# Performance work log

Measured on AMD Instinct MI355X. Metric: run time of the kernel, lower is better.

The kernel has to match this reference:

```python
import jax, jax.numpy as jnp
import numpy as np

N, E, R, D = 50000, 100000, 64, 50


def setup_inputs() -> dict:
    key = jax.random.key(0)
    k0, k1, k2, k3, k4 = jax.random.split(key, 5)
    h = jax.random.normal(k0, (N, D), dtype=jnp.float32)
    # xavier_uniform with gain=sqrt(2) (relu): bound = gain*sqrt(6/(fan_in+fan_out))
    bound = np.sqrt(2.0) * np.sqrt(6.0 / (D + D))
    weight = jax.random.uniform(k1, (R, D, D), dtype=jnp.float32, minval=-bound, maxval=bound)
    bias = jnp.ones((D,), dtype=jnp.float32)
    src_idx = jax.random.randint(k2, (E,), 0, N)
    dst_idx = jax.random.randint(k3, (E,), 0, N)
    rel_type = jax.random.randint(k4, (E,), 0, R)
    return {"h": h, "weight": weight, "bias": bias,
            "src_idx": src_idx, "dst_idx": dst_idx, "rel_type": rel_type}


def reference(h, weight, bias, src_idx, dst_idx, rel_type):
    # message_func: per-edge relation weight gather + bmm with source features
    # h[src_idx]: [E, D], weight[rel_type]: [E, D, D] -> msg: [E, D]
    msg = jnp.einsum('ed,edk->ek', h[src_idx], weight[rel_type])
    # sum-reduce messages onto destination nodes (DGL fn.sum semantics)
    agg = jax.ops.segment_sum(msg, dst_idx, num_segments=N)
    # apply_func: bias add + ReLU on node features
    return jax.nn.relu(agg + bias)
```

## Files before the change

kernel.cpp:

```cpp
#include <hip/hip_runtime.h>

#define NN 50000
#define DD 50
#define RR 64
#define BINS 2048
#define CAP 128
#define CAPN 24

#define BINCUR_OFF 0
#define DCUR_OFF   2048
#define PERM_OFF   52048
#define SD_OFF     1252048
#define META_INTS  1776336
#define WB_BYTE    ((size_t)META_INTS * 4)
#define HB_BYTE    ((WB_BYTE + (size_t)RR * 64 * 64 * 2 + 127) & ~(size_t)127)
#define MSG_BYTE   (HB_BYTE + (size_t)NN * 64 * 2)
#define WS_NEED    (MSG_BYTE + (size_t)BINS * CAP * 64 * 2)

typedef __attribute__((ext_vector_type(8))) short bf16x8;
typedef __attribute__((ext_vector_type(4))) float f32x4;

__device__ __forceinline__ unsigned short f2b(float f) {
    unsigned u = __float_as_uint(f);
    u = (u + 0x7fffu + ((u >> 16) & 1u)) >> 16;
    return (unsigned short)u;
}

__global__ __launch_bounds__(256) void k_init(int* __restrict__ meta,
        unsigned short* __restrict__ wb, unsigned short* __restrict__ hb,
        const float* __restrict__ w, const float* __restrict__ h) {
    int tid = blockIdx.x * 256 + threadIdx.x;
    int nth = gridDim.x * 256;
    for (int j = tid; j < BINS + NN; j += nth) meta[j] = 0;
    for (int j = tid; j < RR * 64 * 64; j += nth) {
        int r = j >> 12, n = (j >> 6) & 63, d = j & 63;
        float v = (n < DD && d < DD) ? w[r * (DD * DD) + d * DD + n] : 0.f;
        wb[j] = f2b(v);
    }
    for (int j = tid; j < NN * 32; j += nth) {
        int n = j >> 5, cp = j & 31;
        unsigned pack = 0;
        if (cp < 25) {
            float2 q = *(const float2*)(h + (size_t)n * DD + cp * 2);
            pack = (unsigned)f2b(q.x) | ((unsigned)f2b(q.y) << 16);
        }
        *(unsigned*)(hb + ((size_t)n << 6) + (cp << 1)) = pack;
    }
}

__global__ void k_scatter(const int* __restrict__ src, const int* __restrict__ dst,
                          const int* __restrict__ rel, int E, int* __restrict__ meta) {
    int e = blockIdx.x * blockDim.x + threadIdx.x;
    if (e >= E) return;
    int sb = (rel[e] << 5) | (e & 31);
    int p = atomicAdd(&meta[BINCUR_OFF + sb], 1);
    if (p < CAP)
        ((int2*)(meta + SD_OFF))[sb * CAP + p] = make_int2(src[e], dst[e]);
}

__global__ __launch_bounds__(256) void k_edge(const unsigned short* __restrict__ hb,
        const unsigned short* __restrict__ wb, int* __restrict__ meta,
        unsigned short* __restrict__ msg) {
    int lane = threadIdx.x & 63;
    int wv = (blockIdx.x << 2) + (threadIdx.x >> 6);
    int b = wv >> 2, qt = wv & 3;
    int cnt = __builtin_amdgcn_readfirstlane(meta[BINCUR_OFF + b]);
    if (cnt > CAP) cnt = CAP;
    int avail = cnt - (qt << 5);
    if (avail <= 0) return;
    if (avail > 32) avail = 32;
    int r = b >> 5;
    int slotbase = (b << 7) + (qt << 5);

    int2 sd = make_int2(0, -1);
    if (lane < avail) sd = ((const int2*)(meta + SD_OFF))[slotbase + lane];
    if (lane < avail) {
        int pos = atomicAdd(&meta[DCUR_OFF + sd.y], 1);
        if (pos < CAPN)
            meta[PERM_OFF + sd.y * CAPN + pos] = slotbase + lane;
    }
    int ch = lane >> 4, col0 = lane & 15;

    int sv0 = __shfl(sd.x, col0);
    int sv1 = __shfl(sd.x, 16 + col0);
    const unsigned short* h0 = hb + ((size_t)sv0 << 6) + (ch << 3);
    const unsigned short* h1 = hb + ((size_t)sv1 << 6) + (ch << 3);
    bf16x8 a00 = *(const bf16x8*)h0;
    bf16x8 a01 = *(const bf16x8*)(h0 + 32);
    bf16x8 a10 = *(const bf16x8*)h1;
    bf16x8 a11 = *(const bf16x8*)(h1 + 32);

    const unsigned short* wr = wb + ((size_t)r << 12) + (col0 << 6) + (ch << 3);
    bf16x8 bb0[4], bb1[4];
    #pragma unroll
    for (int t = 0; t < 4; ++t) {
        bb0[t] = *(const bf16x8*)(wr + t * 1024);
        bb1[t] = *(const bf16x8*)(wr + t * 1024 + 32);
    }

    {
        f32x4 c[4];
        #pragma unroll
        for (int t = 0; t < 4; ++t) {
            c[t] = (f32x4){0.f, 0.f, 0.f, 0.f};
            c[t] = __builtin_amdgcn_mfma_f32_16x16x32_bf16(a00, bb0[t], c[t], 0, 0, 0);
            c[t] = __builtin_amdgcn_mfma_f32_16x16x32_bf16(a01, bb1[t], c[t], 0, 0, 0);
        }
        unsigned short* mb = msg + (size_t)(slotbase + (ch << 2)) * 64;
        #pragma unroll
        for (int q = 0; q < 4; ++q)
            #pragma unroll
            for (int t = 0; t < 4; ++t)
                mb[q * 64 + t * 16 + col0] = f2b(c[t][q]);
    }
    if (avail > 16) {
        f32x4 c[4];
        #pragma unroll
        for (int t = 0; t < 4; ++t) {
            c[t] = (f32x4){0.f, 0.f, 0.f, 0.f};
            c[t] = __builtin_amdgcn_mfma_f32_16x16x32_bf16(a10, bb0[t], c[t], 0, 0, 0);
            c[t] = __builtin_amdgcn_mfma_f32_16x16x32_bf16(a11, bb1[t], c[t], 0, 0, 0);
        }
        unsigned short* mb = msg + (size_t)(slotbase + 16 + (ch << 2)) * 64;
        #pragma unroll
        for (int q = 0; q < 4; ++q)
            #pragma unroll
            for (int t = 0; t < 4; ++t)
                mb[q * 64 + t * 16 + col0] = f2b(c[t][q]);
    }
}

__global__ __launch_bounds__(256) void k_agg(const unsigned short* __restrict__ msg,
        const int* __restrict__ meta, const float* __restrict__ bias,
        float* __restrict__ out) {
    int lane = threadIdx.x & 63;
    int n = (blockIdx.x << 2) + (threadIdx.x >> 6);
    if (n >= NN) return;
    int cnt = __builtin_amdgcn_readfirstlane(meta[DCUR_OFF + n]);
    if (cnt > CAPN) cnt = CAPN;
    float v = 0.f;
    const int4* pp = (const int4*)(meta + PERM_OFF + n * CAPN);
    int4 P0 = pp[0], P1 = pp[1];
    int pj[8] = {P0.x, P0.y, P0.z, P0.w, P1.x, P1.y, P1.z, P1.w};
    #pragma unroll
    for (int j = 0; j < 8; ++j) {
        if (j < cnt) {
            unsigned short u = msg[(size_t)pj[j] * 64 + lane];
            v += __uint_as_float((unsigned)u << 16);
        }
    }
    #pragma unroll 1
    for (int j = 8; j < cnt; ++j) {
        int p = meta[PERM_OFF + n * CAPN + j];
        unsigned short u = msg[(size_t)p * 64 + lane];
        v += __uint_as_float((unsigned)u << 16);
    }
    if (lane < DD) {
        float o = v + bias[lane];
        out[(size_t)n * DD + lane] = o > 0.f ? o : 0.f;
    }
}

__global__ void fb_edge_kernel(const float* __restrict__ h, const float* __restrict__ weight,
                               const int* __restrict__ src_idx, const int* __restrict__ dst_idx,
                               const int* __restrict__ rel_type, float* __restrict__ acc, int E) {
    int wave = (int)((blockIdx.x * blockDim.x + threadIdx.x) >> 6);
    int lane = threadIdx.x & 63;
    if (wave >= E) return;
    int s = src_idx[wave], r = rel_type[wave], dn = dst_idx[wave];
    const float* hs = h + (size_t)s * DD;
    const float* W  = weight + (size_t)r * DD * DD;
    if (lane < DD) {
        float m = 0.f;
        for (int d = 0; d < DD; ++d) m = fmaf(hs[d], W[d * DD + lane], m);
        atomicAdd(&acc[(size_t)dn * DD + lane], m);
    }
}
__global__ void fb_finalize_kernel(float* __restrict__ out, const float* __restrict__ bias, int total) {
    int i = blockIdx.x * blockDim.x + threadIdx.x;
    if (i < total) {
        float v = out[i] + bias[i % DD];
        out[i] = v > 0.f ? v : 0.f;
    }
}

extern "C" void kernel_launch(void* const* d_in, const int* in_sizes, int n_in,
                              void* d_out, int out_size, void* d_ws, size_t ws_size,
                              hipStream_t stream) {
    const float* h      = (const float*)d_in[0];
    const float* weight = (const float*)d_in[1];
    const float* bias   = (const float*)d_in[2];
    const int*   src    = (const int*)d_in[3];
    const int*   dst    = (const int*)d_in[4];
    const int*   rel    = (const int*)d_in[5];
    float* out = (float*)d_out;
    int E = in_sizes[3];

    if (ws_size >= WS_NEED) {
        int* meta = (int*)d_ws;
        unsigned short* wb  = (unsigned short*)((char*)d_ws + WB_BYTE);
        unsigned short* hb  = (unsigned short*)((char*)d_ws + HB_BYTE);
        unsigned short* msg = (unsigned short*)((char*)d_ws + MSG_BYTE);

        k_init<<<2048, 256, 0, stream>>>(meta, wb, hb, weight, h);
        k_scatter<<<(E + 255) / 256, 256, 0, stream>>>(src, dst, rel, E, meta);
        k_edge<<<2048, 256, 0, stream>>>(hb, wb, meta, msg);
        k_agg<<<(NN + 3) / 4, 256, 0, stream>>>(msg, meta, bias, out);
    } else {
        hipMemsetAsync(out, 0, (size_t)out_size * sizeof(float), stream);
        fb_edge_kernel<<<(E + 3) / 4, 256, 0, stream>>>(h, weight, src, dst, rel, out, E);
        fb_finalize_kernel<<<(out_size + 255) / 256, 256, 0, stream>>>(out, bias, out_size);
    }
}
```

Baseline: 56.98 us.

## Drop bf16 copy of node features; convert h on the fly in edge kernel

Removes the pre-pass that converted all node features to a padded bf16 buffer. The edge kernel now reads fp32 rows of h directly and converts them to bf16 in registers. The weight conversion and edge binning are merged into one prep kernel, and counter zeroing moves to a memset. This avoids a full read and write of the feature matrix plus one launch. In exchange, the edge gathers now read twice as many bytes from unaligned fp32 rows and need per-lane bounds checks.

```diff
diff --git a/kernel.cpp b/kernel.cpp
--- a/kernel.cpp
+++ b/kernel.cpp
@@ -13,8 +13,7 @@
 #define SD_OFF     1252048
 #define META_INTS  1776336
 #define WB_BYTE    ((size_t)META_INTS * 4)
-#define HB_BYTE    ((WB_BYTE + (size_t)RR * 64 * 64 * 2 + 127) & ~(size_t)127)
-#define MSG_BYTE   (HB_BYTE + (size_t)NN * 64 * 2)
+#define MSG_BYTE   (WB_BYTE + (size_t)RR * 64 * 64 * 2)
 #define WS_NEED    (MSG_BYTE + (size_t)BINS * CAP * 64 * 2)
 
 typedef __attribute__((ext_vector_type(8))) short bf16x8;
@@ -26,39 +25,42 @@
     return (unsigned short)u;
 }
 
-__global__ __launch_bounds__(256) void k_init(int* __restrict__ meta,
-        unsigned short* __restrict__ wb, unsigned short* __restrict__ hb,
-        const float* __restrict__ w, const float* __restrict__ h) {
+__device__ __forceinline__ void load_a(const float* __restrict__ hrow, int ch,
+                                       bf16x8& a0, bf16x8& a1) {
+    const float2* hp0 = (const float2*)(hrow + ch * 8);
+    float2 q0 = hp0[0], q1 = hp0[1], q2 = hp0[2], q3 = hp0[3];
+    int kb = 32 + ch * 8;
+    const float2 z2 = make_float2(0.f, 0.f);
+    float2 q4 = (kb + 1 < DD) ? *(const float2*)(hrow + kb)     : z2;
+    float2 q5 = (kb + 3 < DD) ? *(const float2*)(hrow + kb + 2) : z2;
+    float2 q6 = (kb + 5 < DD) ? *(const float2*)(hrow + kb + 4) : z2;
+    float2 q7 = (kb + 7 < DD) ? *(const float2*)(hrow + kb + 6) : z2;
+    a0[0] = f2b(q0.x); a0[1] = f2b(q0.y); a0[2] = f2b(q1.x); a0[3] = f2b(q1.y);
+    a0[4] = f2b(q2.x); a0[5] = f2b(q2.y); a0[6] = f2b(q3.x); a0[7] = f2b(q3.y);
+    a1[0] = f2b(q4.x); a1[1] = f2b(q4.y); a1[2] = f2b(q5.x); a1[3] = f2b(q5.y);
+    a1[4] = f2b(q6.x); a1[5] = f2b(q6.y); a1[6] = f2b(q7.x); a1[7] = f2b(q7.y);
+}
+
+__global__ __launch_bounds__(256) void k_prep(int* __restrict__ meta,
+        unsigned short* __restrict__ wb, const float* __restrict__ w,
+        const int* __restrict__ src, const int* __restrict__ dst,
+        const int* __restrict__ rel, int E) {
     int tid = blockIdx.x * 256 + threadIdx.x;
     int nth = gridDim.x * 256;
-    for (int j = tid; j < BINS + NN; j += nth) meta[j] = 0;
     for (int j = tid; j < RR * 64 * 64; j += nth) {
         int r = j >> 12, n = (j >> 6) & 63, d = j & 63;
         float v = (n < DD && d < DD) ? w[r * (DD * DD) + d * DD + n] : 0.f;
         wb[j] = f2b(v);
     }
-    for (int j = tid; j < NN * 32; j += nth) {
-        int n = j >> 5, cp = j & 31;
-        unsigned pack = 0;
-        if (cp < 25) {
-            float2 q = *(const float2*)(h + (size_t)n * DD + cp * 2);
-            pack = (unsigned)f2b(q.x) | ((unsigned)f2b(q.y) << 16);
-        }
-        *(unsigned*)(hb + ((size_t)n << 6) + (cp << 1)) = pack;
-    }
-}
-
-__global__ void k_scatter(const int* __restrict__ src, const int* __restrict__ dst,
-                          const int* __restrict__ rel, int E, int* __restrict__ meta) {
-    int e = blockIdx.x * blockDim.x + threadIdx.x;
-    if (e >= E) return;
-    int sb = (rel[e] << 5) | (e & 31);
-    int p = atomicAdd(&meta[BINCUR_OFF + sb], 1);
-    if (p < CAP)
-        ((int2*)(meta + SD_OFF))[sb * CAP + p] = make_int2(src[e], dst[e]);
-}
-
-__global__ __launch_bounds__(256) void k_edge(const unsigned short* __restrict__ hb,
+    for (int e = tid; e < E; e += nth) {
+        int sb = (rel[e] << 5) | (e & 31);
+        int p = atomicAdd(&meta[BINCUR_OFF + sb], 1);
+        if (p < CAP)
+            ((int2*)(meta + SD_OFF))[sb * CAP + p] = make_int2(src[e], dst[e]);
+    }
+}
+
+__global__ __launch_bounds__(256) void k_edge(const float* __restrict__ h,
         const unsigned short* __restrict__ wb, int* __restrict__ meta,
         unsigned short* __restrict__ msg) {
     int lane = threadIdx.x & 63;
@@ -83,12 +85,9 @@
 
     int sv0 = __shfl(sd.x, col0);
     int sv1 = __shfl(sd.x, 16 + col0);
-    const unsigned short* h0 = hb + ((size_t)sv0 << 6) + (ch << 3);
-    const unsigned short* h1 = hb + ((size_t)sv1 << 6) + (ch << 3);
-    bf16x8 a00 = *(const bf16x8*)h0;
-    bf16x8 a01 = *(const bf16x8*)(h0 + 32);
-    bf16x8 a10 = *(const bf16x8*)h1;
-    bf16x8 a11 = *(const bf16x8*)(h1 + 32);
+    bf16x8 a00, a01, a10, a11;
+    load_a(h + (size_t)sv0 * DD, ch, a00, a01);
+    load_a(h + (size_t)sv1 * DD, ch, a10, a11);
 
     const unsigned short* wr = wb + ((size_t)r << 12) + (col0 << 6) + (ch << 3);
     bf16x8 bb0[4], bb1[4];
@@ -199,12 +198,11 @@
     if (ws_size >= WS_NEED) {
         int* meta = (int*)d_ws;
         unsigned short* wb  = (unsigned short*)((char*)d_ws + WB_BYTE);
-        unsigned short* hb  = (unsigned short*)((char*)d_ws + HB_BYTE);
         unsigned short* msg = (unsigned short*)((char*)d_ws + MSG_BYTE);
 
-        k_init<<<2048, 256, 0, stream>>>(meta, wb, hb, weight, h);
-        k_scatter<<<(E + 255) / 256, 256, 0, stream>>>(src, dst, rel, E, meta);
-        k_edge<<<2048, 256, 0, stream>>>(hb, wb, meta, msg);
+        hipMemsetAsync(meta, 0, (size_t)(BINS + NN) * 4, stream);
+        k_prep<<<1024, 256, 0, stream>>>(meta, wb, weight, src, dst, rel, E);
+        k_edge<<<2048, 256, 0, stream>>>(h, wb, meta, msg);
         k_agg<<<(NN + 3) / 4, 256, 0, stream>>>(msg, meta, bias, out);
     } else {
         hipMemsetAsync(out, 0, (size_t)out_size * sizeof(float), stream);
```

New measurement: 58.37 us. +2.4%, slower.
